# Performance work log

Hardware: AMD Instinct MI355X
Metric: run time of the kernel (lower is better)

## Reference

```python
import jax, jax.numpy as jnp
import numpy as np

B, S, T = 64, 64, 20
E, H, V, K = 512, 1024, 32000, 100
L, W = 50, 8
NEG = -1e9


def lstm_cell(x, h, c, Wih, Whh, bih, bhh):
    # PyTorch gate order: input, forget, cell, output
    g = x @ Wih.T + h @ Whh.T + bih + bhh
    i, f, gg, o = jnp.split(g, 4, axis=-1)
    c = jax.nn.sigmoid(f) * c + jax.nn.sigmoid(i) * jnp.tanh(gg)
    h = jax.nn.sigmoid(o) * jnp.tanh(c)
    return h, c


def setup_inputs():
    key = jax.random.key(0)
    ks = jax.random.split(key, 32)
    rn = lambda k, shp, s=0.02: (s * jax.random.normal(k, shp)).astype(jnp.float32)
    embed_W = jax.random.normal(ks[0], (V, E), dtype=jnp.float32).at[0].set(0.0)  # padding_idx 0
    return {
        'src_seqs': jax.random.randint(ks[1], (B, S), 1, V),
        'src_lengths': jax.random.randint(ks[2], (B,), S // 2, S + 1),
        'trg_seqs': jax.random.randint(ks[3], (B, T), 1, V),
        'ctc_seqs': jax.random.randint(ks[4], (B, L, W), 1, V),
        'ctc_lengths': jax.random.randint(ks[5], (B,), 1, L + 1),
        'embed_W': embed_W,
        'enc_Wih': rn(ks[6], (4 * H, E)), 'enc_Whh': rn(ks[7], (4 * H, H)),
        'enc_bih': rn(ks[8], (4 * H,)), 'enc_bhh': rn(ks[9], (4 * H,)),
        'dec_Wih': rn(ks[10], (4 * H, E + H)), 'dec_Whh': rn(ks[11], (4 * H, H)),
        'dec_bih': rn(ks[12], (4 * H,)), 'dec_bhh': rn(ks[13], (4 * H,)),
        'qk_W': rn(ks[14], (K, E)), 'qk_b': rn(ks[15], (K,)),
        'qv_W': rn(ks[16], (H, E)), 'qv_b': rn(ks[17], (H,)),
        'ak_W': rn(ks[18], (K, H)), 'ak_b': rn(ks[19], (K,)),
        'out_W': rn(ks[20], (E, 2 * H)), 'out_b': rn(ks[21], (E,)),
        'wd_b': rn(ks[22], (V,)),
        'hf1_W': rn(ks[23], (2 * H, H)), 'hf1_b': rn(ks[24], (2 * H,)),
        'hf2_W': rn(ks[25], (H, 2 * H)), 'hf2_b': rn(ks[26], (H,)),
        'cf1_W': rn(ks[27], (2 * H, H)), 'cf1_b': rn(ks[28], (2 * H,)),
        'cf2_W': rn(ks[29], (H, 2 * H)), 'cf2_b': rn(ks[30], (H,)),
    }


def forward(floats, ints):
    (embed_W, enc_Wih, enc_Whh, enc_bih, enc_bhh, dec_Wih, dec_Whh, dec_bih, dec_bhh,
     qk_W, qk_b, qv_W, qv_b, ak_W, ak_b, out_W, out_b, wd_b,
     hf1_W, hf1_b, hf2_W, hf2_b, cf1_W, cf1_b, cf2_W, cf2_b) = floats
    src_seqs, src_lengths, trg_seqs, ctc_seqs, ctc_lengths = ints

    src_embed = embed_W[src_seqs]  # [B,S,E]

    # ---- encoder LSTM (seq-first scan); packed-seq final state = state at src_lengths-1 ----
    def enc_step(carry, x_t):
        h, c = lstm_cell(x_t, carry[0], carry[1], enc_Wih, enc_Whh, enc_bih, enc_bhh)
        return (h, c), (h, c)
    z = jnp.zeros((B, H), jnp.float32)
    _, (hs, cs) = jax.lax.scan(enc_step, (z, z), src_embed.transpose(1, 0, 2))  # [S,B,H]
    idx = src_lengths - 1
    h_last = hs[idx, jnp.arange(B)]
    c_last = cs[idx, jnp.arange(B)]

    # ---- init_hidden: MLP transforms of encoder final state ----
    h0 = jax.nn.relu(h_last @ hf1_W.T + hf1_b) @ hf2_W.T + hf2_b
    c0 = jax.nn.relu(c_last @ cf1_W.T + cf1_b) @ cf2_W.T + cf2_b

    # ---- persona context: mean word embedding per context item ----
    ctx_embed = embed_W[ctc_seqs].mean(axis=2)       # [B,L,E]
    q_key = jnp.tanh(ctx_embed @ qk_W.T + qk_b)      # [B,L,K]
    q_value = ctx_embed @ qv_W.T + qv_b              # [B,L,H]
    mask = jnp.arange(L)[None, :] < ctc_lengths[:, None]  # [B,L]

    ans_embed = embed_W[trg_seqs]                    # [B,T,E]

    # ---- decoder: per-step attention + LSTM + tied-vocab projection ----
    def dec_step(carry, x_t):
        h, c = carry
        a_key = jnp.tanh(h @ ak_W.T + ak_b)                      # [B,K]
        e = jnp.einsum('blk,bk->bl', q_key, a_key)
        w = jax.nn.softmax(jnp.where(mask, e, NEG), axis=1)
        ctx = jnp.einsum('bl,blh->bh', w, q_value)               # [B,H]
        h, c = lstm_cell(jnp.concatenate([x_t, ctx], -1), h, c,
                         dec_Wih, dec_Whh, dec_bih, dec_bhh)
        ox = jnp.concatenate([h, ctx], -1) @ out_W.T + out_b     # [B,E]
        logits = ox @ embed_W.T + wd_b                           # tied weights, [B,V]
        return (h, c), logits

    # teacher forcing (sampling_rate=1.0, T-1 <= max_len-2)
    _, logits = jax.lax.scan(dec_step, (h0, c0), ans_embed[:, :T - 1].transpose(1, 0, 2))
    return logits.transpose(1, 0, 2)  # [B, T-1, V]


def reference(src_seqs, src_lengths, trg_seqs, ctc_seqs, ctc_lengths, embed_W, enc_Wih, enc_Whh, enc_bih, enc_bhh, dec_Wih, dec_Whh, dec_bih, dec_bhh, qk_W, qk_b, qv_W, qv_b, ak_W, ak_b, out_W, out_b, wd_b, hf1_W, hf1_b, hf2_W, hf2_b, cf1_W, cf1_b, cf2_W, cf2_b):
    floats = (embed_W, enc_Wih, enc_Whh, enc_bih, enc_bhh, dec_Wih, dec_Whh, dec_bih, dec_bhh,
              qk_W, qk_b, qv_W, qv_b, ak_W, ak_b, out_W, out_b, wd_b,
              hf1_W, hf1_b, hf2_W, hf2_b, cf1_W, cf1_b, cf2_W, cf2_b)
    ints = (src_seqs, src_lengths, trg_seqs, ctc_seqs, ctc_lengths)
    return forward(floats, ints)
```

## Files before the change

kernel.cpp:

```cpp
#include <hip/hip_runtime.h>
#include <hip/hip_bf16.h>
#include <math.h>

#define Bn 64
#define Sn 64
#define Tn 20
#define TD 19
#define En 512
#define Hn 1024
#define Vn 32000
#define Kan 100
#define Lnn 50
#define Wnn 8

typedef __attribute__((ext_vector_type(8))) short short8v;
typedef __attribute__((ext_vector_type(4))) float floatx4;
typedef __hip_bfloat16 bf16;

__device__ __forceinline__ float sigm(float x) { return 1.0f / (1.0f + expf(-x)); }

#define EOFF(r, p) (((r) << 5) + ((((p) ^ ((r) & 3))) << 3))

template<int GATHER, int EPI, int ACT>
__global__ __launch_bounds__(256)
void mgemm(const bf16* __restrict__ A, int lda, const int* __restrict__ tok,
           const bf16* __restrict__ W, int ldw,
           const float* __restrict__ b1, const float* __restrict__ b2,
           float* __restrict__ C, int ldc,
           bf16* __restrict__ Cbf, int ldcbf,
           int M, int N, int K)
{
    __shared__ bf16 As[128 * 32];
    __shared__ bf16 Bs[128 * 32];
    const int tid = threadIdx.x;
    const int lane = tid & 63, wv = tid >> 6;
    const int wm = wv >> 1, wn = wv & 1;
    const int r0 = blockIdx.y * 128, n0 = blockIdx.x * 128;
    const int srow = tid >> 2, sp = tid & 3;

    const int ra_r0 = r0 + srow, ra_r1 = r0 + srow + 64;
    const bool av0 = ra_r0 < M, av1 = ra_r1 < M;
    const size_t arow0 = (size_t)(av0 ? (GATHER ? tok[ra_r0] : ra_r0) : 0) * lda;
    const size_t arow1 = (size_t)(av1 ? (GATHER ? tok[ra_r1] : ra_r1) : 0) * lda;
    const size_t wrow0 = (size_t)(n0 + srow) * ldw;
    const size_t wrow1 = (size_t)(n0 + srow + 64) * ldw;

    const uint4 z4 = make_uint4(0, 0, 0, 0);
    uint4 ra0, ra1, rb0, rb1;
#define LOADTILE_G(k0) do { \
        ra0 = av0 ? *((const uint4*)(A + arow0 + (k0)) + sp) : z4; \
        ra1 = av1 ? *((const uint4*)(A + arow1 + (k0)) + sp) : z4; \
        rb0 = *((const uint4*)(W + wrow0 + (k0)) + sp); \
        rb1 = *((const uint4*)(W + wrow1 + (k0)) + sp); \
    } while (0)

    floatx4 acc[4][4] = {};
    const int lr = lane & 15, p2 = lane >> 4;

    LOADTILE_G(0);
    for (int k0 = 0; k0 < K; k0 += 32) {
        __syncthreads();
        *(uint4*)(As + EOFF(srow, sp)) = ra0;
        *(uint4*)(As + EOFF(srow + 64, sp)) = ra1;
        *(uint4*)(Bs + EOFF(srow, sp)) = rb0;
        *(uint4*)(Bs + EOFF(srow + 64, sp)) = rb1;
        __syncthreads();
        if (k0 + 32 < K) LOADTILE_G(k0 + 32);
        short8v aF[4], bF[4];
#pragma unroll
        for (int mf = 0; mf < 4; ++mf)
            aF[mf] = *(const short8v*)(As + EOFF(wm * 64 + mf * 16 + lr, p2));
#pragma unroll
        for (int nf = 0; nf < 4; ++nf)
            bF[nf] = *(const short8v*)(Bs + EOFF(wn * 64 + nf * 16 + lr, p2));
#pragma unroll
        for (int mf = 0; mf < 4; ++mf)
#pragma unroll
            for (int nf = 0; nf < 4; ++nf)
                acc[mf][nf] = __builtin_amdgcn_mfma_f32_16x16x32_bf16(
                    aF[mf], bF[nf], acc[mf][nf], 0, 0, 0);
    }
#undef LOADTILE_G

    const int rbase = r0 + wm * 64 + (lane >> 4) * 4;
    const int nbase = n0 + wn * 64 + (lane & 15);
#pragma unroll
    for (int nf = 0; nf < 4; ++nf) {
        const int n = nbase + nf * 16;
        if (n >= N) continue;
        float bias = b1 ? b1[n] : 0.0f;
        if (b2) bias += b2[n];
#pragma unroll
        for (int mf = 0; mf < 4; ++mf) {
#pragma unroll
            for (int i = 0; i < 4; ++i) {
                const int r = rbase + mf * 16 + i;
                if (r >= M) continue;
                float v = acc[mf][nf][i] + bias;
                if (ACT == 1) v = tanhf(v);
                if (ACT == 2) v = fmaxf(v, 0.0f);
                if (EPI == 2) {
                    int b = r & 63, t = r >> 6;
                    C[(size_t)(b * TD + t) * Vn + n] = v;
                } else {
                    if (C) C[(size_t)r * ldc + n] = v;
                    if (Cbf) Cbf[(size_t)r * ldcbf + n] = __float2bfloat16(v);
                }
            }
        }
    }
}

__global__ __launch_bounds__(256)
void lstm_mfma(const bf16* __restrict__ Ah, int lda,
               const bf16* __restrict__ Wp,
               const bf16* __restrict__ Xg,
               const float* __restrict__ cprev, float* __restrict__ cnext,
               float* __restrict__ hfp,
               bf16* __restrict__ hbf, int ldhbf,
               bf16* __restrict__ hbf2,
               const int* __restrict__ lengths, int t,
               float* __restrict__ hlast, float* __restrict__ clast,
               int K)
{
    __shared__ bf16 As[64 * 32];
    __shared__ bf16 Bs[128 * 32];
    __shared__ float Gs[64][133];
    const int tid = threadIdx.x;
    const int lane = tid & 63, wn = tid >> 6;
    const int n0 = blockIdx.x * 128;
    const int srow = tid >> 2, sp = tid & 3;

    const size_t arow = (size_t)srow * lda;
    const size_t wrow0 = (size_t)(n0 + srow) * K;
    const size_t wrow1 = (size_t)(n0 + srow + 64) * K;

    uint4 ra0, rb0, rb1;
#define LOADTILE_L(k0) do { \
        ra0 = *((const uint4*)(Ah + arow + (k0)) + sp); \
        rb0 = *((const uint4*)(Wp + wrow0 + (k0)) + sp); \
        rb1 = *((const uint4*)(Wp + wrow1 + (k0)) + sp); \
    } while (0)

    floatx4 acc[4][2] = {};
    const int lr = lane & 15, p2 = lane >> 4;

    LOADTILE_L(0);
    for (int k0 = 0; k0 < K; k0 += 32) {
        __syncthreads();
        *(uint4*)(As + EOFF(srow, sp)) = ra0;
        *(uint4*)(Bs + EOFF(srow, sp)) = rb0;
        *(uint4*)(Bs + EOFF(srow + 64, sp)) = rb1;
        __syncthreads();
        if (k0 + 32 < K) LOADTILE_L(k0 + 32);
        short8v aF[4], bF[2];
#pragma unroll
        for (int mf = 0; mf < 4; ++mf)
            aF[mf] = *(const short8v*)(As + EOFF(mf * 16 + lr, p2));
#pragma unroll
        for (int nf = 0; nf < 2; ++nf)
            bF[nf] = *(const short8v*)(Bs + EOFF(wn * 32 + nf * 16 + lr, p2));
#pragma unroll
        for (int mf = 0; mf < 4; ++mf)
#pragma unroll
            for (int nf = 0; nf < 2; ++nf)
                acc[mf][nf] = __builtin_amdgcn_mfma_f32_16x16x32_bf16(
                    aF[mf], bF[nf], acc[mf][nf], 0, 0, 0);
    }
#undef LOADTILE_L

#pragma unroll
    for (int mf = 0; mf < 4; ++mf)
#pragma unroll
        for (int nf = 0; nf < 2; ++nf)
#pragma unroll
            for (int i = 0; i < 4; ++i)
                Gs[(lane >> 4) * 4 + i + mf * 16][wn * 32 + nf * 16 + (lane & 15)] =
                    acc[mf][nf][i];
    __syncthreads();

#pragma unroll
    for (int it = 0; it < 8; ++it) {
        int cell = tid + it * 256;
        int jl = cell & 31, b = cell >> 5;
        int j = (n0 >> 2) + jl;
        const bf16* xg = Xg + (size_t)b * 4096;
        float gi = Gs[b][jl * 4 + 0] + __bfloat162float(xg[j]);
        float gf = Gs[b][jl * 4 + 1] + __bfloat162float(xg[1024 + j]);
        float gg = Gs[b][jl * 4 + 2] + __bfloat162float(xg[2048 + j]);
        float go = Gs[b][jl * 4 + 3] + __bfloat162float(xg[3072 + j]);
        float cp = cprev[b * 1024 + j];
        float cnv = sigm(gf) * cp + sigm(gi) * tanhf(gg);
        float hnv = sigm(go) * tanhf(cnv);
        cnext[b * 1024 + j] = cnv;
        hbf[(size_t)b * ldhbf + j] = __float2bfloat16(hnv);
        if (hfp) hfp[b * 1024 + j] = hnv;
        if (hbf2) hbf2[(size_t)b * 2048 + j] = __float2bfloat16(hnv);
        if (lengths && t == lengths[b] - 1) {
            hlast[b * 1024 + j] = hnv;
            clast[b * 1024 + j] = cnv;
        }
    }
}

__global__ __launch_bounds__(256)
void attn_kernel(const float* __restrict__ h,
                 const float* __restrict__ akW, const float* __restrict__ akb,
                 const float* __restrict__ qkey,
                 const float* __restrict__ qval,
                 const int* __restrict__ clen,
                 bf16* __restrict__ ctx1,
                 bf16* __restrict__ ctx2)
{
    const int b = blockIdx.x;
    const int tid = threadIdx.x;
    const int lane = tid & 63, wv = tid >> 6;
    __shared__ float hsh[1024];
    __shared__ float akey[104];
    __shared__ float wts[52];

#pragma unroll
    for (int p = 0; p < 4; ++p) hsh[tid + p * 256] = h[(size_t)b * Hn + tid + p * 256];
    __syncthreads();

    for (int k = wv; k < Kan; k += 4) {
        float s = 0.0f;
#pragma unroll
        for (int m = 0; m < 16; ++m)
            s += hsh[lane + m * 64] * akW[(size_t)k * Hn + lane + m * 64];
        for (int off = 32; off; off >>= 1) s += __shfl_down(s, off);
        if (lane == 0) akey[k] = tanhf(s + akb[k]);
    }
    __syncthreads();

    if (wv == 0) {
        float e;
        int len = clen[b];
        if (lane < Lnn) {
            if (lane < len) {
                float s = 0.0f;
                const float* qr = qkey + (size_t)(b * Lnn + lane) * Kan;
                for (int k = 0; k < Kan; ++k) s += qr[k] * akey[k];
                e = s;
            } else {
                e = -1e9f;
            }
        } else {
            e = -3.402823466e38f;
        }
        float mx = e;
        for (int off = 32; off; off >>= 1) mx = fmaxf(mx, __shfl_xor(mx, off));
        float p = (lane < Lnn) ? expf(e - mx) : 0.0f;
        float sm = p;
        for (int off = 32; off; off >>= 1) sm += __shfl_xor(sm, off);
        if (lane < Lnn) wts[lane] = p / sm;
    }
    __syncthreads();

#pragma unroll
    for (int p = 0; p < 4; ++p) {
        int j = tid + p * 256;
        float s = 0.0f;
        for (int l = 0; l < Lnn; ++l)
            s += wts[l] * qval[((size_t)b * Lnn + l) * Hn + j];
        bf16 v = __float2bfloat16(s);
        ctx1[(size_t)b * 2048 + j] = v;
        ctx2[(size_t)b * 2048 + j] = v;
    }
}

__global__ __launch_bounds__(128)
void ctx_embed_kernel(const int* __restrict__ ctc, const float* __restrict__ embed,
                      bf16* __restrict__ ctxe_bf)
{
    const int row = blockIdx.x;
    const int tid = threadIdx.x;
    __shared__ int toks[8];
    if (tid < 8) toks[tid] = ctc[row * Wnn + tid];
    __syncthreads();
#pragma unroll
    for (int p = 0; p < 4; ++p) {
        int e = tid + p * 128;
        float s = 0.0f;
#pragma unroll
        for (int w = 0; w < 8; ++w) s += embed[(size_t)toks[w] * En + e];
        ctxe_bf[(size_t)row * En + e] = __float2bfloat16(s * 0.125f);
    }
}

__global__ void prep_tokens(const int* __restrict__ src, const int* __restrict__ trg,
                            int* __restrict__ tokA, int* __restrict__ tokD)
{
    int i = blockIdx.x * 256 + threadIdx.x;
    if (i < Bn * Sn) tokA[i] = src[(i & 63) * Sn + (i >> 6)];
    if (i < TD * Bn) tokD[i] = trg[(i & 63) * Tn + (i >> 6)];
}

__global__ void conv_f2b(const float* __restrict__ src, bf16* __restrict__ dst, int n)
{
    int i = (blockIdx.x * 256 + threadIdx.x) * 4;
    if (i >= n) return;
    float4 v = *(const float4*)(src + i);
    dst[i + 0] = __float2bfloat16(v.x);
    dst[i + 1] = __float2bfloat16(v.y);
    dst[i + 2] = __float2bfloat16(v.z);
    dst[i + 3] = __float2bfloat16(v.w);
}

__global__ void pad_qkw(const float* __restrict__ qkW, bf16* __restrict__ Wp)
{
    int i = blockIdx.x * 256 + threadIdx.x;
    int r = i >> 9;
    Wp[i] = __float2bfloat16(r < Kan ? qkW[(size_t)r * En + (i & 511)] : 0.0f);
}

__global__ void perm_enc(const float* __restrict__ Whh, bf16* __restrict__ Wp)
{
    int row = blockIdx.x;
    int j = row >> 2, g = row & 3;
    const float* s = Whh + (size_t)(g * 1024 + j) * 1024;
    bf16* d = Wp + (size_t)row * 1024;
    for (int e = threadIdx.x; e < 1024; e += 256) d[e] = __float2bfloat16(s[e]);
}

__global__ void perm_dec(const float* __restrict__ Whh, const float* __restrict__ Wih,
                         bf16* __restrict__ Wp)
{
    int row = blockIdx.x;
    int j = row >> 2, g = row & 3;
    int sr = g * 1024 + j;
    const float* s1 = Whh + (size_t)sr * 1024;
    const float* s2 = Wih + (size_t)sr * 1536 + 512;
    bf16* d = Wp + (size_t)row * 2048;
    for (int e = threadIdx.x; e < 1024; e += 256) {
        d[e] = __float2bfloat16(s1[e]);
        d[1024 + e] = __float2bfloat16(s2[e]);
    }
}

extern "C" void kernel_launch(void* const* d_in, const int* in_sizes, int n_in,
                              void* d_out, int out_size, void* d_ws, size_t ws_size,
                              hipStream_t stream)
{
    (void)in_sizes; (void)n_in; (void)out_size; (void)ws_size;
    const int*   src     = (const int*)d_in[0];
    const int*   srclen  = (const int*)d_in[1];
    const int*   trg     = (const int*)d_in[2];
    const int*   ctc     = (const int*)d_in[3];
    const int*   ctclen  = (const int*)d_in[4];
    const float* embed   = (const float*)d_in[5];
    const float* enc_Wih = (const float*)d_in[6];
    const float* enc_Whh = (const float*)d_in[7];
    const float* enc_bih = (const float*)d_in[8];
    const float* enc_bhh = (const float*)d_in[9];
    const float* dec_Wih = (const float*)d_in[10];
    const float* dec_Whh = (const float*)d_in[11];
    const float* dec_bih = (const float*)d_in[12];
    const float* dec_bhh = (const float*)d_in[13];
    const float* qkW     = (const float*)d_in[14];
    const float* qkb     = (const float*)d_in[15];
    const float* qvW     = (const float*)d_in[16];
    const float* qvb     = (const float*)d_in[17];
    const float* akW     = (const float*)d_in[18];
    const float* akb     = (const float*)d_in[19];
    const float* outW    = (const float*)d_in[20];
    const float* outb    = (const float*)d_in[21];
    const float* wdb     = (const float*)d_in[22];
    const float* hf1W    = (const float*)d_in[23];
    const float* hf1b    = (const float*)d_in[24];
    const float* hf2W    = (const float*)d_in[25];
    const float* hf2b    = (const float*)d_in[26];
    const float* cf1W    = (const float*)d_in[27];
    const float* cf1b    = (const float*)d_in[28];
    const float* cf2W    = (const float*)d_in[29];
    const float* cf2b    = (const float*)d_in[30];
    float* out = (float*)d_out;

    char* ws = (char*)d_ws;
    size_t off = 0;
    auto alloc = [&](size_t bytes) -> void* {
        void* p = ws + off;
        off += (bytes + 255) & ~(size_t)255;
        return p;
    };
    bf16*  embed_bf  = (bf16*)alloc((size_t)Vn * En * 2);
    bf16*  encWih_bf = (bf16*)alloc((size_t)4096 * En * 2);
    bf16*  decWih_bf = (bf16*)alloc((size_t)4096 * 1536 * 2);
    bf16*  qvW_bf    = (bf16*)alloc((size_t)Hn * En * 2);
    bf16*  outW_bf   = (bf16*)alloc((size_t)En * 2048 * 2);
    bf16*  Wenc_p    = (bf16*)alloc((size_t)4096 * 1024 * 2);
    bf16*  Wdec_p    = (bf16*)alloc((size_t)4096 * 2048 * 2);
    bf16*  hf1W_bf   = (bf16*)alloc((size_t)2048 * 1024 * 2);
    bf16*  hf2W_bf   = (bf16*)alloc((size_t)1024 * 2048 * 2);
    bf16*  cf1W_bf   = (bf16*)alloc((size_t)2048 * 1024 * 2);
    bf16*  cf2W_bf   = (bf16*)alloc((size_t)1024 * 2048 * 2);
    bf16*  qkWp      = (bf16*)alloc((size_t)128 * En * 2);
    bf16*  Xenc_bf   = (bf16*)alloc((size_t)Sn * Bn * 4096 * 2);
    bf16*  Xdec_bf   = (bf16*)alloc((size_t)TD * Bn * 4096 * 2);
    float* qkey      = (float*)alloc((size_t)Bn * Lnn * Kan * 4);
    float* qval      = (float*)alloc((size_t)Bn * Lnn * Hn * 4);
    bf16*  ctxe_bf   = (bf16*)alloc((size_t)Bn * Lnn * En * 2);
    bf16*  a2e0      = (bf16*)alloc((size_t)Bn * 1024 * 2);
    bf16*  a2e1      = (bf16*)alloc((size_t)Bn * 1024 * 2);
    bf16*  a2d0      = (bf16*)alloc((size_t)Bn * 2048 * 2);
    bf16*  a2d1      = (bf16*)alloc((size_t)Bn * 2048 * 2);
    float* cbuf0     = (float*)alloc((size_t)Bn * Hn * 4);
    float* cbuf1     = (float*)alloc((size_t)Bn * Hn * 4);
    float* hbd0      = (float*)alloc((size_t)Bn * Hn * 4);
    float* hbd1      = (float*)alloc((size_t)Bn * Hn * 4);
    float* hlast     = (float*)alloc((size_t)Bn * Hn * 4);
    float* clast     = (float*)alloc((size_t)Bn * Hn * 4);
    bf16*  hlast_bf  = (bf16*)alloc((size_t)Bn * Hn * 2);
    bf16*  clast_bf  = (bf16*)alloc((size_t)Bn * Hn * 2);
    bf16*  t2h_bf    = (bf16*)alloc((size_t)Bn * 2048 * 2);
    bf16*  t2c_bf    = (bf16*)alloc((size_t)Bn * 2048 * 2);
    int*   tokA      = (int*)alloc((size_t)Bn * Sn * 4);
    int*   tokD      = (int*)alloc((size_t)TD * Bn * 4);
    bf16*  hcat_bf   = Xenc_bf;
    bf16*  ox_bf     = Xenc_bf + (size_t)TD * Bn * 2048;

    conv_f2b<<<(Vn * En) / 1024, 256, 0, stream>>>(embed, embed_bf, Vn * En);
    conv_f2b<<<(4096 * En) / 1024, 256, 0, stream>>>(enc_Wih, encWih_bf, 4096 * En);
    conv_f2b<<<(4096 * 1536) / 1024, 256, 0, stream>>>(dec_Wih, decWih_bf, 4096 * 1536);
    conv_f2b<<<(Hn * En) / 1024, 256, 0, stream>>>(qvW, qvW_bf, Hn * En);
    conv_f2b<<<(En * 2048) / 1024, 256, 0, stream>>>(outW, outW_bf, En * 2048);
    conv_f2b<<<(2048 * 1024) / 1024, 256, 0, stream>>>(hf1W, hf1W_bf, 2048 * 1024);
    conv_f2b<<<(1024 * 2048) / 1024, 256, 0, stream>>>(hf2W, hf2W_bf, 1024 * 2048);
    conv_f2b<<<(2048 * 1024) / 1024, 256, 0, stream>>>(cf1W, cf1W_bf, 2048 * 1024);
    conv_f2b<<<(1024 * 2048) / 1024, 256, 0, stream>>>(cf2W, cf2W_bf, 1024 * 2048);
    pad_qkw<<<(128 * En) / 256, 256, 0, stream>>>(qkW, qkWp);
    perm_enc<<<4096, 256, 0, stream>>>(enc_Whh, Wenc_p);
    perm_dec<<<4096, 256, 0, stream>>>(dec_Whh, dec_Wih, Wdec_p);
    prep_tokens<<<16, 256, 0, stream>>>(src, trg, tokA, tokD);
    ctx_embed_kernel<<<Bn * Lnn, 128, 0, stream>>>(ctc, embed, ctxe_bf);

    mgemm<1, 0, 0><<<dim3(32, 32), 256, 0, stream>>>(
        embed_bf, En, tokA, encWih_bf, En, enc_bih, enc_bhh,
        nullptr, 0, Xenc_bf, 4096, Bn * Sn, 4096, En);
    mgemm<1, 0, 0><<<dim3(32, 10), 256, 0, stream>>>(
        embed_bf, En, tokD, decWih_bf, 1536, dec_bih, dec_bhh,
        nullptr, 0, Xdec_bf, 4096, TD * Bn, 4096, En);
    mgemm<0, 0, 0><<<dim3(8, 25), 256, 0, stream>>>(
        ctxe_bf, En, nullptr, qvW_bf, En, qvb, nullptr,
        qval, Hn, nullptr, 0, Bn * Lnn, Hn, En);
    mgemm<0, 0, 1><<<dim3(1, 25), 256, 0, stream>>>(
        ctxe_bf, En, nullptr, qkWp, En, qkb, nullptr,
        qkey, Kan, nullptr, 0, Bn * Lnn, Kan, En);

    hipMemsetAsync(a2e0, 0, (size_t)Bn * 1024 * 2, stream);
    hipMemsetAsync(cbuf0, 0, (size_t)Bn * Hn * 4, stream);

    bf16*  a2e[2] = {a2e0, a2e1};
    bf16*  a2d[2] = {a2d0, a2d1};
    float* cb[2]  = {cbuf0, cbuf1};
    float* hbd[2] = {hbd0, hbd1};

    for (int t = 0; t < Sn; ++t) {
        lstm_mfma<<<32, 256, 0, stream>>>(
            a2e[t & 1], 1024, Wenc_p, Xenc_bf + (size_t)t * Bn * 4096,
            cb[t & 1], cb[(t + 1) & 1],
            nullptr, a2e[(t + 1) & 1], 1024, nullptr,
            srclen, t, hlast, clast, 1024);
    }

    conv_f2b<<<(Bn * Hn) / 1024, 256, 0, stream>>>(hlast, hlast_bf, Bn * Hn);
    conv_f2b<<<(Bn * Hn) / 1024, 256, 0, stream>>>(clast, clast_bf, Bn * Hn);
    mgemm<0, 0, 2><<<dim3(16, 1), 256, 0, stream>>>(
        hlast_bf, Hn, nullptr, hf1W_bf, Hn, hf1b, nullptr,
        nullptr, 0, t2h_bf, 2048, Bn, 2048, Hn);
    mgemm<0, 0, 0><<<dim3(8, 1), 256, 0, stream>>>(
        t2h_bf, 2048, nullptr, hf2W_bf, 2048, hf2b, nullptr,
        hbd0, Hn, a2d0, 2048, Bn, Hn, 2048);
    mgemm<0, 0, 2><<<dim3(16, 1), 256, 0, stream>>>(
        clast_bf, Hn, nullptr, cf1W_bf, Hn, cf1b, nullptr,
        nullptr, 0, t2c_bf, 2048, Bn, 2048, Hn);
    mgemm<0, 0, 0><<<dim3(8, 1), 256, 0, stream>>>(
        t2c_bf, 2048, nullptr, cf2W_bf, 2048, cf2b, nullptr,
        cbuf0, Hn, nullptr, 0, Bn, Hn, 2048);

    for (int t = 0; t < TD; ++t) {
        bf16* hcat_t = hcat_bf + (size_t)t * Bn * 2048;
        attn_kernel<<<Bn, 256, 0, stream>>>(
            hbd[t & 1], akW, akb, qkey, qval, ctclen,
            a2d[t & 1] + 1024, hcat_t + 1024);
        lstm_mfma<<<32, 256, 0, stream>>>(
            a2d[t & 1], 2048, Wdec_p, Xdec_bf + (size_t)t * Bn * 4096,
            cb[t & 1], cb[(t + 1) & 1],
            hbd[(t + 1) & 1], a2d[(t + 1) & 1], 2048, hcat_t,
            nullptr, 0, nullptr, nullptr, 2048);
    }

    mgemm<0, 0, 0><<<dim3(4, 10), 256, 0, stream>>>(
        hcat_bf, 2048, nullptr, outW_bf, 2048, outb, nullptr,
        nullptr, 0, ox_bf, En, TD * Bn, En, 2048);
    mgemm<0, 2, 0><<<dim3(Vn / 128, 10), 256, 0, stream>>>(
        ox_bf, En, nullptr, embed_bf, En, wdb, nullptr,
        out, 0, nullptr, 0, TD * Bn, Vn, En);
}
```

Baseline: 2.903 ms.

## Replace per-step LSTM launches with persistent cooperative encoder and decoder kernels

The encoder and decoder recurrences become two persistent cooperative kernels of 128 blocks. Each block keeps its 32-column slice of the recurrent weights resident in LDS (swizzled), holds the cell state in registers, and steps time with grid.sync. Attention is folded into the decoder kernel, so the roughly 100 per-step kernel launches and the repeated weight reloads from global memory go away. The vocab GEMM grid is also transposed so that blocks sharing an embedding tile run together. The trade-offs are grid-wide barrier cost, a single wave of 512-thread blocks doing small MFMA work per step, and a dependence on all blocks being co-resident.

Result: slower. 3.169 ms (+9.2%).

```diff
diff --git a/kernel.cpp b/kernel.cpp
--- a/kernel.cpp
+++ b/kernel.cpp
@@ -1,6 +1,9 @@
 #include <hip/hip_runtime.h>
 #include <hip/hip_bf16.h>
+#include <hip/hip_cooperative_groups.h>
 #include <math.h>
+
+namespace cg = cooperative_groups;
 
 #define Bn 64
 #define Sn 64
@@ -21,6 +24,13 @@
 
 #define EOFF(r, p) (((r) << 5) + ((((p) ^ ((r) & 3))) << 3))
 
+__device__ __forceinline__ int aswz(int row, int p) {
+    return row * 32 + (((p ^ ((row >> 1) & 3))) << 3);
+}
+__device__ __forceinline__ int wswz(int col, int s, int K) {
+    return col * K + (((s & ~7) | ((s & 7) ^ (col & 7))) << 3);
+}
+
 template<int GATHER, int EPI, int ACT>
 __global__ __launch_bounds__(256)
 void mgemm(const bf16* __restrict__ A, int lda, const int* __restrict__ tok,
@@ -35,7 +45,8 @@
     const int tid = threadIdx.x;
     const int lane = tid & 63, wv = tid >> 6;
     const int wm = wv >> 1, wn = wv & 1;
-    const int r0 = blockIdx.y * 128, n0 = blockIdx.x * 128;
+    const int n0 = (EPI == 2 ? blockIdx.y : blockIdx.x) * 128;
+    const int r0 = (EPI == 2 ? blockIdx.x : blockIdx.y) * 128;
     const int srow = tid >> 2, sp = tid & 3;
 
     const int ra_r0 = r0 + srow, ra_r1 = r0 + srow + 64;
@@ -111,161 +122,233 @@
     }
 }
 
-__global__ __launch_bounds__(256)
-void lstm_mfma(const bf16* __restrict__ Ah, int lda,
-               const bf16* __restrict__ Wp,
-               const bf16* __restrict__ Xg,
-               const float* __restrict__ cprev, float* __restrict__ cnext,
-               float* __restrict__ hfp,
-               bf16* __restrict__ hbf, int ldhbf,
-               bf16* __restrict__ hbf2,
-               const int* __restrict__ lengths, int t,
-               float* __restrict__ hlast, float* __restrict__ clast,
-               int K)
-{
-    __shared__ bf16 As[64 * 32];
-    __shared__ bf16 Bs[128 * 32];
-    __shared__ float Gs[64][133];
+struct EncP {
+    const bf16* Wp;
+    const bf16* Xg;
+    bf16* hA; bf16* hB;
+    const int* len;
+    bf16* hlast; bf16* clast;
+};
+
+__global__ __launch_bounds__(512, 1)
+void enc_persist(EncP p)
+{
+    __shared__ bf16 Ws_l[32 * 1024];
+    __shared__ bf16 Asb[2][64 * 32];
+    __shared__ float Gs[64][33];
     const int tid = threadIdx.x;
-    const int lane = tid & 63, wn = tid >> 6;
-    const int n0 = blockIdx.x * 128;
+    const int lane = tid & 63, wv = tid >> 6;
+    const int mf = wv >> 1, nf = wv & 1;
+    const int n0 = blockIdx.x * 32;
+
+    for (int idx = tid; idx < 32 * 128; idx += 512) {
+        int col = idx >> 7, s = idx & 127;
+        uint4 v = *(const uint4*)(p.Wp + (size_t)(n0 + col) * 1024 + s * 8);
+        *(uint4*)(Ws_l + wswz(col, s, 1024)) = v;
+    }
+
+    const int b = tid >> 3, jl = tid & 7;
+    const int j = (n0 >> 2) + jl;
+    float c_reg = 0.0f;
+    p.hA[b * 1024 + j] = __float2bfloat16(0.0f);
+    const int mylen = p.len[b];
+
+    const int arow = mf * 16 + (lane & 15);
+    const int a_rd = aswz(arow, lane >> 4);
+    const int bcol = nf * 16 + (lane & 15);
+    const int bbase = bcol * 1024;
     const int srow = tid >> 2, sp = tid & 3;
-
-    const size_t arow = (size_t)srow * lda;
-    const size_t wrow0 = (size_t)(n0 + srow) * K;
-    const size_t wrow1 = (size_t)(n0 + srow + 64) * K;
-
-    uint4 ra0, rb0, rb1;
-#define LOADTILE_L(k0) do { \
-        ra0 = *((const uint4*)(Ah + arow + (k0)) + sp); \
-        rb0 = *((const uint4*)(Wp + wrow0 + (k0)) + sp); \
-        rb1 = *((const uint4*)(Wp + wrow1 + (k0)) + sp); \
-    } while (0)
-
-    floatx4 acc[4][2] = {};
-    const int lr = lane & 15, p2 = lane >> 4;
-
-    LOADTILE_L(0);
-    for (int k0 = 0; k0 < K; k0 += 32) {
+    const int a_wr = aswz(srow, sp);
+    const int gr = mf * 16 + (lane >> 4) * 4;
+    const int gc = nf * 16 + (lane & 15);
+
+    cg::grid_group grid = cg::this_grid();
+    grid.sync();
+
+    for (int t = 0; t < Sn; ++t) {
+        const bf16* hp = (t & 1) ? p.hB : p.hA;
+        bf16* hn = (t & 1) ? p.hA : p.hB;
+        floatx4 acc = {};
+        uint4 ra;
+        if (tid < 256) ra = *(const uint4*)(hp + srow * 1024 + sp * 8);
         __syncthreads();
-        *(uint4*)(As + EOFF(srow, sp)) = ra0;
-        *(uint4*)(Bs + EOFF(srow, sp)) = rb0;
-        *(uint4*)(Bs + EOFF(srow + 64, sp)) = rb1;
+        if (tid < 256) *(uint4*)(Asb[0] + a_wr) = ra;
+        if (tid < 256) ra = *(const uint4*)(hp + srow * 1024 + 32 + sp * 8);
+        for (int k0 = 0; k0 < 1024; k0 += 32) {
+            const int cur = (k0 >> 5) & 1;
+            __syncthreads();
+            if (k0 + 32 < 1024) {
+                if (tid < 256) *(uint4*)(Asb[cur ^ 1] + a_wr) = ra;
+                if (k0 + 64 < 1024 && tid < 256)
+                    ra = *(const uint4*)(hp + srow * 1024 + k0 + 64 + sp * 8);
+            }
+            short8v af = *(const short8v*)(Asb[cur] + a_rd);
+            int s = (k0 >> 3) + (lane >> 4);
+            short8v bfr = *(const short8v*)(Ws_l + bbase +
+                             (((s & ~7) | ((s & 7) ^ (bcol & 7))) << 3));
+            acc = __builtin_amdgcn_mfma_f32_16x16x32_bf16(af, bfr, acc, 0, 0, 0);
+        }
+        Gs[gr + 0][gc] = acc[0];
+        Gs[gr + 1][gc] = acc[1];
+        Gs[gr + 2][gc] = acc[2];
+        Gs[gr + 3][gc] = acc[3];
         __syncthreads();
-        if (k0 + 32 < K) LOADTILE_L(k0 + 32);
-        short8v aF[4], bF[2];
-#pragma unroll
-        for (int mf = 0; mf < 4; ++mf)
-            aF[mf] = *(const short8v*)(As + EOFF(mf * 16 + lr, p2));
-#pragma unroll
-        for (int nf = 0; nf < 2; ++nf)
-            bF[nf] = *(const short8v*)(Bs + EOFF(wn * 32 + nf * 16 + lr, p2));
-#pragma unroll
-        for (int mf = 0; mf < 4; ++mf)
-#pragma unroll
-            for (int nf = 0; nf < 2; ++nf)
-                acc[mf][nf] = __builtin_amdgcn_mfma_f32_16x16x32_bf16(
-                    aF[mf], bF[nf], acc[mf][nf], 0, 0, 0);
-    }
-#undef LOADTILE_L
-
-#pragma unroll
-    for (int mf = 0; mf < 4; ++mf)
-#pragma unroll
-        for (int nf = 0; nf < 2; ++nf)
-#pragma unroll
-            for (int i = 0; i < 4; ++i)
-                Gs[(lane >> 4) * 4 + i + mf * 16][wn * 32 + nf * 16 + (lane & 15)] =
-                    acc[mf][nf][i];
-    __syncthreads();
-
-#pragma unroll
-    for (int it = 0; it < 8; ++it) {
-        int cell = tid + it * 256;
-        int jl = cell & 31, b = cell >> 5;
-        int j = (n0 >> 2) + jl;
-        const bf16* xg = Xg + (size_t)b * 4096;
+        const bf16* xg = p.Xg + ((size_t)t * Bn + b) * 4096;
         float gi = Gs[b][jl * 4 + 0] + __bfloat162float(xg[j]);
         float gf = Gs[b][jl * 4 + 1] + __bfloat162float(xg[1024 + j]);
         float gg = Gs[b][jl * 4 + 2] + __bfloat162float(xg[2048 + j]);
         float go = Gs[b][jl * 4 + 3] + __bfloat162float(xg[3072 + j]);
-        float cp = cprev[b * 1024 + j];
-        float cnv = sigm(gf) * cp + sigm(gi) * tanhf(gg);
+        float cnv = sigm(gf) * c_reg + sigm(gi) * tanhf(gg);
         float hnv = sigm(go) * tanhf(cnv);
-        cnext[b * 1024 + j] = cnv;
-        hbf[(size_t)b * ldhbf + j] = __float2bfloat16(hnv);
-        if (hfp) hfp[b * 1024 + j] = hnv;
-        if (hbf2) hbf2[(size_t)b * 2048 + j] = __float2bfloat16(hnv);
-        if (lengths && t == lengths[b] - 1) {
-            hlast[b * 1024 + j] = hnv;
-            clast[b * 1024 + j] = cnv;
+        c_reg = cnv;
+        bf16 hb = __float2bfloat16(hnv);
+        hn[b * 1024 + j] = hb;
+        if (t == mylen - 1) {
+            p.hlast[b * 1024 + j] = hb;
+            p.clast[b * 1024 + j] = __float2bfloat16(cnv);
         }
-    }
-}
-
-__global__ __launch_bounds__(256)
-void attn_kernel(const float* __restrict__ h,
-                 const float* __restrict__ akW, const float* __restrict__ akb,
-                 const float* __restrict__ qkey,
-                 const float* __restrict__ qval,
-                 const int* __restrict__ clen,
-                 bf16* __restrict__ ctx1,
-                 bf16* __restrict__ ctx2)
-{
-    const int b = blockIdx.x;
+        grid.sync();
+    }
+}
+
+struct DecP {
+    const bf16* Wp;
+    const bf16* Xg;
+    bf16* hA; bf16* hB;
+    bf16* ctx;
+    const float* c0;
+    const float* akW; const float* akb;
+    const float* qkey;
+    const float* qval;
+    const int* clen;
+    bf16* hcat;
+};
+
+__global__ __launch_bounds__(512, 1)
+void dec_persist(DecP p)
+{
+    __shared__ bf16 Ws_l[32 * 2048];
+    __shared__ bf16 Asb[2][64 * 32];
+    __shared__ float Gs[64][33];
+    __shared__ float akey[104];
+    __shared__ float wts[52];
+    float* hsh = &Gs[0][0];
+
     const int tid = threadIdx.x;
     const int lane = tid & 63, wv = tid >> 6;
-    __shared__ float hsh[1024];
-    __shared__ float akey[104];
-    __shared__ float wts[52];
-
-#pragma unroll
-    for (int p = 0; p < 4; ++p) hsh[tid + p * 256] = h[(size_t)b * Hn + tid + p * 256];
-    __syncthreads();
-
-    for (int k = wv; k < Kan; k += 4) {
-        float s = 0.0f;
-#pragma unroll
-        for (int m = 0; m < 16; ++m)
-            s += hsh[lane + m * 64] * akW[(size_t)k * Hn + lane + m * 64];
-        for (int off = 32; off; off >>= 1) s += __shfl_down(s, off);
-        if (lane == 0) akey[k] = tanhf(s + akb[k]);
-    }
-    __syncthreads();
-
-    if (wv == 0) {
-        float e;
-        int len = clen[b];
-        if (lane < Lnn) {
-            if (lane < len) {
+    const int mf = wv >> 1, nf = wv & 1;
+    const int n0 = blockIdx.x * 32;
+
+    for (int idx = tid; idx < 32 * 256; idx += 512) {
+        int col = idx >> 8, s = idx & 255;
+        uint4 v = *(const uint4*)(p.Wp + (size_t)(n0 + col) * 2048 + s * 8);
+        *(uint4*)(Ws_l + wswz(col, s, 2048)) = v;
+    }
+
+    const int b = tid >> 3, jl = tid & 7;
+    const int j = (n0 >> 2) + jl;
+    float c_reg = p.c0[b * 1024 + j];
+
+    const int arow = mf * 16 + (lane & 15);
+    const int a_rd = aswz(arow, lane >> 4);
+    const int bcol = nf * 16 + (lane & 15);
+    const int bbase = bcol * 2048;
+    const int srow = tid >> 2, sp = tid & 3;
+    const int a_wr = aswz(srow, sp);
+    const int gr = mf * 16 + (lane >> 4) * 4;
+    const int gc = nf * 16 + (lane & 15);
+
+    cg::grid_group grid = cg::this_grid();
+    grid.sync();
+
+    for (int t = 0; t < TD; ++t) {
+        const bf16* hp = (t & 1) ? p.hB : p.hA;
+        bf16* hn = (t & 1) ? p.hA : p.hB;
+
+        if (blockIdx.x < 64) {
+            const int ab = blockIdx.x;
+            for (int i = tid; i < 1024; i += 512)
+                hsh[i] = __bfloat162float(hp[ab * 1024 + i]);
+            __syncthreads();
+            for (int k = wv; k < Kan; k += 8) {
                 float s = 0.0f;
-                const float* qr = qkey + (size_t)(b * Lnn + lane) * Kan;
-                for (int k = 0; k < Kan; ++k) s += qr[k] * akey[k];
-                e = s;
-            } else {
-                e = -1e9f;
+#pragma unroll
+                for (int m = 0; m < 16; ++m)
+                    s += hsh[lane + m * 64] * p.akW[(size_t)k * 1024 + lane + m * 64];
+                for (int off = 32; off; off >>= 1) s += __shfl_down(s, off);
+                if (lane == 0) akey[k] = tanhf(s + p.akb[k]);
             }
-        } else {
-            e = -3.402823466e38f;
+            __syncthreads();
+            if (wv == 0) {
+                float e;
+                int len = p.clen[ab];
+                if (lane < Lnn) {
+                    if (lane < len) {
+                        float s = 0.0f;
+                        const float* qr = p.qkey + (size_t)(ab * Lnn + lane) * Kan;
+                        for (int k = 0; k < Kan; ++k) s += qr[k] * akey[k];
+                        e = s;
+                    } else e = -1e9f;
+                } else e = -3.402823466e38f;
+                float mx = e;
+                for (int off = 32; off; off >>= 1) mx = fmaxf(mx, __shfl_xor(mx, off));
+                float pr = (lane < Lnn) ? expf(e - mx) : 0.0f;
+                float sm = pr;
+                for (int off = 32; off; off >>= 1) sm += __shfl_xor(sm, off);
+                if (lane < Lnn) wts[lane] = pr / sm;
+            }
+            __syncthreads();
+            for (int jj = tid; jj < 1024; jj += 512) {
+                float s = 0.0f;
+                for (int l = 0; l < Lnn; ++l)
+                    s += wts[l] * p.qval[((size_t)ab * Lnn + l) * 1024 + jj];
+                bf16 v = __float2bfloat16(s);
+                p.ctx[ab * 1024 + jj] = v;
+                p.hcat[((size_t)t * Bn + ab) * 2048 + 1024 + jj] = v;
+            }
         }
-        float mx = e;
-        for (int off = 32; off; off >>= 1) mx = fmaxf(mx, __shfl_xor(mx, off));
-        float p = (lane < Lnn) ? expf(e - mx) : 0.0f;
-        float sm = p;
-        for (int off = 32; off; off >>= 1) sm += __shfl_xor(sm, off);
-        if (lane < Lnn) wts[lane] = p / sm;
-    }
-    __syncthreads();
-
-#pragma unroll
-    for (int p = 0; p < 4; ++p) {
-        int j = tid + p * 256;
-        float s = 0.0f;
-        for (int l = 0; l < Lnn; ++l)
-            s += wts[l] * qval[((size_t)b * Lnn + l) * Hn + j];
-        bf16 v = __float2bfloat16(s);
-        ctx1[(size_t)b * 2048 + j] = v;
-        ctx2[(size_t)b * 2048 + j] = v;
+        grid.sync();
+
+        floatx4 acc = {};
+        uint4 ra;
+        if (tid < 256) ra = *(const uint4*)(hp + srow * 1024 + sp * 8);
+        __syncthreads();
+        if (tid < 256) *(uint4*)(Asb[0] + a_wr) = ra;
+        if (tid < 256) ra = *(const uint4*)(hp + srow * 1024 + 32 + sp * 8);
+        for (int k0 = 0; k0 < 2048; k0 += 32) {
+            const int cur = (k0 >> 5) & 1;
+            __syncthreads();
+            if (k0 + 32 < 2048) {
+                if (tid < 256) *(uint4*)(Asb[cur ^ 1] + a_wr) = ra;
+                if (k0 + 64 < 2048 && tid < 256) {
+                    const int kn = k0 + 64;
+                    const bf16* asrc = (kn < 1024) ? hp : p.ctx;
+                    ra = *(const uint4*)(asrc + srow * 1024 + (kn & 1023) + sp * 8);
+                }
+            }
+            short8v af = *(const short8v*)(Asb[cur] + a_rd);
+            int s = (k0 >> 3) + (lane >> 4);
+            short8v bfr = *(const short8v*)(Ws_l + bbase +
+                             (((s & ~7) | ((s & 7) ^ (bcol & 7))) << 3));
+            acc = __builtin_amdgcn_mfma_f32_16x16x32_bf16(af, bfr, acc, 0, 0, 0);
+        }
+        Gs[gr + 0][gc] = acc[0];
+        Gs[gr + 1][gc] = acc[1];
+        Gs[gr + 2][gc] = acc[2];
+        Gs[gr + 3][gc] = acc[3];
+        __syncthreads();
+        const bf16* xg = p.Xg + ((size_t)t * Bn + b) * 4096;
+        float gi = Gs[b][jl * 4 + 0] + __bfloat162float(xg[j]);
+        float gf = Gs[b][jl * 4 + 1] + __bfloat162float(xg[1024 + j]);
+        float gg = Gs[b][jl * 4 + 2] + __bfloat162float(xg[2048 + j]);
+        float go = Gs[b][jl * 4 + 3] + __bfloat162float(xg[3072 + j]);
+        float cnv = sigm(gf) * c_reg + sigm(gi) * tanhf(gg);
+        float hnv = sigm(go) * tanhf(cnv);
+        c_reg = cnv;
+        bf16 hb = __float2bfloat16(hnv);
+        hn[b * 1024 + j] = hb;
+        p.hcat[((size_t)t * Bn + b) * 2048 + j] = hb;
+        grid.sync();
     }
 }
 
@@ -400,16 +483,12 @@
     float* qkey      = (float*)alloc((size_t)Bn * Lnn * Kan * 4);
     float* qval      = (float*)alloc((size_t)Bn * Lnn * Hn * 4);
     bf16*  ctxe_bf   = (bf16*)alloc((size_t)Bn * Lnn * En * 2);
-    bf16*  a2e0      = (bf16*)alloc((size_t)Bn * 1024 * 2);
-    bf16*  a2e1      = (bf16*)alloc((size_t)Bn * 1024 * 2);
-    bf16*  a2d0      = (bf16*)alloc((size_t)Bn * 2048 * 2);
-    bf16*  a2d1      = (bf16*)alloc((size_t)Bn * 2048 * 2);
+    bf16*  henc0     = (bf16*)alloc((size_t)Bn * Hn * 2);
+    bf16*  henc1     = (bf16*)alloc((size_t)Bn * Hn * 2);
+    bf16*  hdec0     = (bf16*)alloc((size_t)Bn * Hn * 2);
+    bf16*  hdec1     = (bf16*)alloc((size_t)Bn * Hn * 2);
+    bf16*  ctxbuf    = (bf16*)alloc((size_t)Bn * Hn * 2);
     float* cbuf0     = (float*)alloc((size_t)Bn * Hn * 4);
-    float* cbuf1     = (float*)alloc((size_t)Bn * Hn * 4);
-    float* hbd0      = (float*)alloc((size_t)Bn * Hn * 4);
-    float* hbd1      = (float*)alloc((size_t)Bn * Hn * 4);
-    float* hlast     = (float*)alloc((size_t)Bn * Hn * 4);
-    float* clast     = (float*)alloc((size_t)Bn * Hn * 4);
     bf16*  hlast_bf  = (bf16*)alloc((size_t)Bn * Hn * 2);
     bf16*  clast_bf  = (bf16*)alloc((size_t)Bn * Hn * 2);
     bf16*  t2h_bf    = (bf16*)alloc((size_t)Bn * 2048 * 2);
@@ -447,30 +526,21 @@
         ctxe_bf, En, nullptr, qkWp, En, qkb, nullptr,
         qkey, Kan, nullptr, 0, Bn * Lnn, Kan, En);
 
-    hipMemsetAsync(a2e0, 0, (size_t)Bn * 1024 * 2, stream);
-    hipMemsetAsync(cbuf0, 0, (size_t)Bn * Hn * 4, stream);
-
-    bf16*  a2e[2] = {a2e0, a2e1};
-    bf16*  a2d[2] = {a2d0, a2d1};
-    float* cb[2]  = {cbuf0, cbuf1};
-    float* hbd[2] = {hbd0, hbd1};
-
-    for (int t = 0; t < Sn; ++t) {
-        lstm_mfma<<<32, 256, 0, stream>>>(
-            a2e[t & 1], 1024, Wenc_p, Xenc_bf + (size_t)t * Bn * 4096,
-            cb[t & 1], cb[(t + 1) & 1],
-            nullptr, a2e[(t + 1) & 1], 1024, nullptr,
-            srclen, t, hlast, clast, 1024);
-    }
-
-    conv_f2b<<<(Bn * Hn) / 1024, 256, 0, stream>>>(hlast, hlast_bf, Bn * Hn);
-    conv_f2b<<<(Bn * Hn) / 1024, 256, 0, stream>>>(clast, clast_bf, Bn * Hn);
+    {
+        EncP ep;
+        ep.Wp = Wenc_p; ep.Xg = Xenc_bf; ep.hA = henc0; ep.hB = henc1;
+        ep.len = srclen; ep.hlast = hlast_bf; ep.clast = clast_bf;
+        void* args[] = {&ep};
+        hipLaunchCooperativeKernel((void*)enc_persist, dim3(128), dim3(512),
+                                   args, 0, stream);
+    }
+
     mgemm<0, 0, 2><<<dim3(16, 1), 256, 0, stream>>>(
         hlast_bf, Hn, nullptr, hf1W_bf, Hn, hf1b, nullptr,
         nullptr, 0, t2h_bf, 2048, Bn, 2048, Hn);
     mgemm<0, 0, 0><<<dim3(8, 1), 256, 0, stream>>>(
         t2h_bf, 2048, nullptr, hf2W_bf, 2048, hf2b, nullptr,
-        hbd0, Hn, a2d0, 2048, Bn, Hn, 2048);
+        nullptr, 0, hdec0, 1024, Bn, Hn, 2048);
     mgemm<0, 0, 2><<<dim3(16, 1), 256, 0, stream>>>(
         clast_bf, Hn, nullptr, cf1W_bf, Hn, cf1b, nullptr,
         nullptr, 0, t2c_bf, 2048, Bn, 2048, Hn);
@@ -478,22 +548,21 @@
         t2c_bf, 2048, nullptr, cf2W_bf, 2048, cf2b, nullptr,
         cbuf0, Hn, nullptr, 0, Bn, Hn, 2048);
 
-    for (int t = 0; t < TD; ++t) {
-        bf16* hcat_t = hcat_bf + (size_t)t * Bn * 2048;
-        attn_kernel<<<Bn, 256, 0, stream>>>(
-            hbd[t & 1], akW, akb, qkey, qval, ctclen,
-            a2d[t & 1] + 1024, hcat_t + 1024);
-        lstm_mfma<<<32, 256, 0, stream>>>(
-            a2d[t & 1], 2048, Wdec_p, Xdec_bf + (size_t)t * Bn * 4096,
-            cb[t & 1], cb[(t + 1) & 1],
-            hbd[(t + 1) & 1], a2d[(t + 1) & 1], 2048, hcat_t,
-            nullptr, 0, nullptr, nullptr, 2048);
+    {
+        DecP dp;
+        dp.Wp = Wdec_p; dp.Xg = Xdec_bf; dp.hA = hdec0; dp.hB = hdec1;
+        dp.ctx = ctxbuf; dp.c0 = cbuf0;
+        dp.akW = akW; dp.akb = akb; dp.qkey = qkey; dp.qval = qval;
+        dp.clen = ctclen; dp.hcat = hcat_bf;
+        void* args[] = {&dp};
+        hipLaunchCooperativeKernel((void*)dec_persist, dim3(128), dim3(512),
+                                   args, 0, stream);
     }
 
     mgemm<0, 0, 0><<<dim3(4, 10), 256, 0, stream>>>(
         hcat_bf, 2048, nullptr, outW_bf, 2048, outb, nullptr,
         nullptr, 0, ox_bf, En, TD * Bn, En, 2048);
-    mgemm<0, 2, 0><<<dim3(Vn / 128, 10), 256, 0, stream>>>(
+    mgemm<0, 2, 0><<<dim3(10, Vn / 128), 256, 0, stream>>>(
         ox_bf, En, nullptr, embed_bf, En, wdb, nullptr,
         out, 0, nullptr, 0, TD * Bn, Vn, En);
 }
```
